# Kernel optimization log

Hardware: AMD Instinct MI355X
Metric: run time of the kernel (lower is better)

Reference implementation:

```python
import jax, jax.numpy as jnp
import numpy as np

B, N, C = 64, 16384, 3
NUM_PATCHES, PATCH_POINTS, EMBED_DIM = 64, 32, 384
BN_EPS = 1e-5


def farthest_point_sample(xyz, npoint):
    # xyz: (B, N, 3) -> (B, npoint) int32 indices. Deterministic start at index 0
    # (torch version uses a random start point).
    b, n, _ = xyz.shape
    bidx = jnp.arange(b)

    def step(carry, _):
        distance, farthest = carry
        centroid = xyz[bidx, farthest][:, None, :]          # (B,1,3)
        d = jnp.sum((xyz - centroid) ** 2, -1)              # (B,N)
        distance = jnp.minimum(distance, d)
        nxt = jnp.argmax(distance, -1).astype(jnp.int32)
        return (distance, nxt), farthest

    init = (jnp.full((b, n), 1e10, xyz.dtype), jnp.zeros((b,), jnp.int32))
    _, cent = jax.lax.scan(step, init, None, length=npoint)
    return jnp.transpose(cent)                               # (B, npoint)


def query_ball(xyz, new_xyz, nsample):
    # nsample nearest neighbors by squared distance (radius arg is unused in source).
    sq = (jnp.sum(new_xyz ** 2, -1)[:, :, None]
          + jnp.sum(xyz ** 2, -1)[:, None, :]
          - 2.0 * jnp.einsum('bsc,bnc->bsn', new_xyz, xyz))  # (B,S,N)
    _, idx = jax.lax.top_k(-sq, nsample)                     # smallest distances
    return idx                                               # (B,S,K)


def batchnorm(h, g, b):
    # training-mode BN over (batch*patches, points) per channel (last axis)
    m = jnp.mean(h, axis=(0, 1, 2))
    v = jnp.mean((h - m) ** 2, axis=(0, 1, 2))
    return (h - m) * jax.lax.rsqrt(v + BN_EPS) * g + b


def setup_inputs() -> dict:
    key = jax.random.key(0)
    ks = jax.random.split(key, 4)
    x = jax.random.normal(ks[0], (B, N, C), jnp.float32)
    W1 = jax.random.normal(ks[1], (64, C), jnp.float32) * (1.0 / np.sqrt(C))
    W2 = jax.random.normal(ks[2], (128, 64), jnp.float32) * (1.0 / np.sqrt(64))
    W3 = jax.random.normal(ks[3], (EMBED_DIM, 128), jnp.float32) * (1.0 / np.sqrt(128))
    return dict(
        x=x,
        W1=W1, b1=jnp.zeros((64,), jnp.float32),
        g1=jnp.ones((64,), jnp.float32), be1=jnp.zeros((64,), jnp.float32),
        W2=W2, b2=jnp.zeros((128,), jnp.float32),
        g2=jnp.ones((128,), jnp.float32), be2=jnp.zeros((128,), jnp.float32),
        W3=W3, b3=jnp.zeros((EMBED_DIM,), jnp.float32),
    )


def reference(x, W1, b1, g1, be1, W2, b2, g2, be2, W3, b3):
    b = x.shape[0]
    bidx2 = jnp.arange(b)[:, None]
    bidx3 = jnp.arange(b)[:, None, None]

    fps_idx = farthest_point_sample(x[:, :, :3], NUM_PATCHES)   # (B,S)
    centers = x[bidx2, fps_idx][:, :, :3]                       # (B,S,3)
    idx = query_ball(x[:, :, :3], centers, PATCH_POINTS)        # (B,S,K)
    patches = x[bidx3, idx]                                     # (B,S,K,C)
    patches = jnp.concatenate(
        [patches[..., :3] - centers[:, :, None, :], patches[..., 3:]], axis=-1)

    h = jnp.einsum('bskc,oc->bsko', patches, W1) + b1           # (B,S,K,64)
    h = jax.nn.relu(batchnorm(h, g1, be1))
    h = jnp.einsum('bsko,po->bskp', h, W2) + b2                 # (B,S,K,128)
    h = jax.nn.relu(batchnorm(h, g2, be2))
    h = jnp.einsum('bskp,ep->bske', h, W3) + b3                 # (B,S,K,384)
    embeddings = jnp.max(h, axis=2)                             # (B,S,384)
    return embeddings, centers
```

## Files before the change

kernel.cpp:

```cpp
#include <hip/hip_runtime.h>
#include <hip/hip_bf16.h>

#define B_  64
#define N_  16384
#define S_  64
#define K_  32
#define C1_ 64
#define C2_ 128
#define C3_ 384
#define R_  (B_*S_*K_)
#define BN_EPS_ 1e-5f

#define PATCH_OFF 0
#define CENT_OFF  (R_*3)
#define NB1_ 512
#define P1_OFF    (CENT_OFF + B_*S_*3)
#define SC1_OFF   (P1_OFF + NB1_*C1_*2)
#define NB2_ 512
#define P2_OFF    (SC1_OFF + 2*C1_)
#define SC2_OFF   (P2_OFF + NB2_*C2_*2)
#define W2BF_OFF  (SC2_OFF + 2*C2_)
#define W3BF_OFF  (W2BF_OFF + 4096)

#define MOMB_ 48

typedef short bf16x8 __attribute__((ext_vector_type(8)));
typedef float f32x4  __attribute__((ext_vector_type(4)));

static __device__ __forceinline__ unsigned short f2bf(float f) {
  unsigned u = __float_as_uint(f);
  unsigned r = (u + 0x7fffu + ((u >> 16) & 1u)) >> 16;
  return (unsigned short)r;
}

static __device__ __forceinline__ unsigned fToKey(float d) {
  unsigned u = __float_as_uint(d);
  return (u & 0x80000000u) ? ~u : (u | 0x80000000u);
}
static __device__ __forceinline__ float keyToF(unsigned k) {
  return (k & 0x80000000u) ? __uint_as_float(k & 0x7fffffffu)
                           : -__uint_as_float(~k);
}

__global__ void prep_kernel(const float* __restrict__ W2, const float* __restrict__ W3,
                            short* __restrict__ w2bf, short* __restrict__ w3bf) {
  int i = blockIdx.x * 256 + threadIdx.x;
  if (i < C2_*C1_) w2bf[i] = (short)f2bf(W2[i]);
  int j = i - C2_*C1_;
  if (j >= 0 && j < C3_*C2_) w3bf[j] = (short)f2bf(W3[j]);
}

__global__ __launch_bounds__(1024, 4) void fps_kernel(const float* __restrict__ x,
        float* __restrict__ centers, float* __restrict__ outCent) {
  int b = blockIdx.x;
  int t = threadIdx.x;
  const float* xb = x + (size_t)b * N_ * 3;
  float px[16], py[16], pz[16], dist[16];
#pragma unroll
  for (int j = 0; j < 16; ++j) {
    int n = j * 1024 + t;
    px[j] = xb[n*3+0]; py[j] = xb[n*3+1]; pz[j] = xb[n*3+2];
    dist[j] = 1e10f;
  }
  __shared__ float wd[2][16];
  __shared__ int   wi[2][16];
  float cx = xb[0], cy = xb[1], cz = xb[2];
  int lane = t & 63, wv = t >> 6;
  for (int s = 0; s < S_; ++s) {
    if (t == 0) {
      int task = b * S_ + s;
      centers[task*3+0] = cx; centers[task*3+1] = cy; centers[task*3+2] = cz;
      outCent[task*3+0] = cx; outCent[task*3+1] = cy; outCent[task*3+2] = cz;
    }
    float bd = -1.0f; int bn = 0;
#pragma unroll
    for (int j = 0; j < 16; ++j) {
      float dx = px[j]-cx, dy = py[j]-cy, dz = pz[j]-cz;
      float d = __builtin_fmaf(dz, dz, __builtin_fmaf(dy, dy, dx*dx));
      float dm = fminf(dist[j], d);
      dist[j] = dm;
      int n = j*1024 + t;
      if (dm > bd) { bd = dm; bn = n; }
    }
#pragma unroll
    for (int m = 1; m < 64; m <<= 1) {
      float od = __shfl_xor(bd, m, 64); int on = __shfl_xor(bn, m, 64);
      if (od > bd || (od == bd && on < bn)) { bd = od; bn = on; }
    }
    int buf = s & 1;
    if (lane == 0) { wd[buf][wv] = bd; wi[buf][wv] = bn; }
    __syncthreads();
    float vd = wd[buf][lane & 15];
    int   vi = wi[buf][lane & 15];
#pragma unroll
    for (int m = 1; m < 16; m <<= 1) {
      float od = __shfl_xor(vd, m, 64); int oi = __shfl_xor(vi, m, 64);
      if (od > vd || (od == vd && oi < vi)) { vd = od; vi = oi; }
    }
    int gn = vi;
    cx = xb[gn*3+0]; cy = xb[gn*3+1]; cz = xb[gn*3+2];
  }
}

__global__ __launch_bounds__(512, 4) void qb_kernel(const float* __restrict__ x,
        const float* __restrict__ centers, float* __restrict__ patches) {
  int t = threadIdx.x;
  int lane = t & 63, wv = t >> 6;
  int task = blockIdx.x;
  int b = task >> 6;
  const float* xb = x + (size_t)b * N_ * 3;
  float cx = centers[task*3+0], cy = centers[task*3+1], cz = centers[task*3+2];
  float A = __builtin_fmaf(cz, cz, __builtin_fmaf(cy, cy, cx*cx));

  __shared__ unsigned long long buf64[8][128];
  __shared__ unsigned long long wtop64[256];
  __shared__ int winIdx[32];
  __shared__ int sortedIdx[32];

  unsigned key[32];
  unsigned kmin = 0xffffffffu;
#pragma unroll
  for (int j = 0; j < 32; ++j) {
    int n = j * 512 + t;
    float qx = xb[n*3+0], qy = xb[n*3+1], qz = xb[n*3+2];
    float Bn = __builtin_fmaf(qz, qz, __builtin_fmaf(qy, qy, qx*qx));
    float dt = __builtin_fmaf(cz, qz, __builtin_fmaf(cy, qy, cx*qx));
    float d  = __builtin_fmaf(-2.0f, dt, A + Bn);
    unsigned u = __float_as_uint(d);
    unsigned k = (u & 0x80000000u) ? ~u : (u | 0x80000000u);
    key[j] = k;
    kmin = min(kmin, k);
  }
#pragma unroll
  for (int m = 1; m < 64; m <<= 1)
    kmin = min(kmin, (unsigned)__shfl_xor((int)kmin, m, 64));
  unsigned T0 = key[0];
#pragma unroll
  for (int m = 1; m < 64; m <<= 1)
    T0 = min(T0, (unsigned)__shfl_xor((int)T0, m, 64));

  unsigned Tcur = T0;
  int c;
  {
    int cc = 0;
#pragma unroll
    for (int j = 0; j < 32; ++j) cc += (key[j] < Tcur) ? 1 : 0;
#pragma unroll
    for (int m = 1; m < 64; m <<= 1) cc += __shfl_xor(cc, m, 64);
    c = cc;
  }
  float dmin = keyToF(kmin);
  for (int iter = 0; iter < 4 && !(c >= 32 && c <= 128); ++iter) {
    float dcur = keyToF(Tcur);
    if (!(dcur > dmin)) break;
    float cf = fmaxf((float)c, 1.0f);
    float ratio = exp2f(0.66666667f * log2f(64.0f / cf));
    float dnew = dmin + (dcur - dmin) * ratio;
    unsigned Tn = fToKey(dnew);
    if (Tn == Tcur) break;
    Tcur = Tn;
    int cc = 0;
#pragma unroll
    for (int j = 0; j < 32; ++j) cc += (key[j] < Tcur) ? 1 : 0;
#pragma unroll
    for (int m = 1; m < 64; m <<= 1) cc += __shfl_xor(cc, m, 64);
    c = cc;
  }

  int cW = 0;
  if (c >= 32 && c <= 128) {
    int base = 0;
#pragma unroll
    for (int j = 0; j < 32; ++j) {
      bool p = key[j] < Tcur;
      unsigned long long mk = __ballot(p);
      if (p) {
        int pos = base + (int)__popcll(mk & ((1ull << lane) - 1ull));
        buf64[wv][pos] = ((unsigned long long)key[j] << 32) | (unsigned)(j*512 + t);
      }
      base += (int)__popcll(mk);
    }
    cW = base;
  } else {
    unsigned a = 0xffffffffu, o = 0u;
#pragma unroll
    for (int j = 0; j < 32; ++j) { a &= key[j]; o |= key[j]; }
#pragma unroll
    for (int m = 1; m < 64; m <<= 1) {
      a &= (unsigned)__shfl_xor((int)a, m, 64);
      o |= (unsigned)__shfl_xor((int)o, m, 64);
    }
    unsigned diff = a ^ o;
    unsigned result = 0u, CAND = 0u;
    bool early = false;
    for (int bit = 31; bit >= 0; --bit) {
      unsigned msk = 1u << bit;
      if (!(diff & msk)) { result |= (a & msk); continue; }
      unsigned tryv = result | msk;
      int cc = 0;
#pragma unroll
      for (int j = 0; j < 32; ++j) cc += (key[j] < tryv) ? 1 : 0;
#pragma unroll
      for (int m = 1; m < 64; m <<= 1) cc += __shfl_xor(cc, m, 64);
      if (cc >= 32 && cc <= 128) { early = true; CAND = tryv; break; }
      if (cc < 32) result = tryv;
    }
    if (early) {
      int base = 0;
#pragma unroll
      for (int j = 0; j < 32; ++j) {
        bool p = key[j] < CAND;
        unsigned long long mk = __ballot(p);
        if (p) {
          int pos = base + (int)__popcll(mk & ((1ull << lane) - 1ull));
          buf64[wv][pos] = ((unsigned long long)key[j] << 32) | (unsigned)(j*512 + t);
        }
        base += (int)__popcll(mk);
      }
      cW = base;
    } else {
      unsigned T = result;
      int base = 0;
#pragma unroll
      for (int j = 0; j < 32; ++j) {
        bool p = key[j] < T;
        unsigned long long mk = __ballot(p);
        if (p) {
          int pos = base + (int)__popcll(mk & ((1ull << lane) - 1ull));
          buf64[wv][pos] = ((unsigned long long)key[j] << 32) | (unsigned)(j*512 + t);
        }
        base += (int)__popcll(mk);
      }
      int cl = base;
      int picked = -1;
      for (int r = 0; r < 32 - cl; ++r) {
        int cand = 0x7fffffff;
#pragma unroll
        for (int j = 0; j < 32; ++j) {
          int n = j*512 + t;
          if (key[j] == T && n > picked && n < cand) cand = n;
        }
#pragma unroll
        for (int m = 1; m < 64; m <<= 1) cand = min(cand, __shfl_xor(cand, m, 64));
        if (lane == 0)
          buf64[wv][cl + r] = ((unsigned long long)T << 32) | (unsigned)cand;
        picked = cand;
      }
      cW = 32;
    }
  }

  {
    unsigned long long my0 = (lane < cW) ? buf64[wv][lane] : ~0ull;
    unsigned long long my1 = (lane + 64 < cW) ? buf64[wv][lane + 64] : ~0ull;
    int r0 = 0, r1 = 0;
    for (int jj = 0; jj < cW; ++jj) {
      unsigned long long ov = buf64[wv][jj];
      r0 += (ov < my0) ? 1 : 0;
      r1 += (ov < my1) ? 1 : 0;
    }
    if (lane < cW && r0 < 32) wtop64[wv*32 + r0] = my0;
    if (lane + 64 < cW && r1 < 32) wtop64[wv*32 + r1] = my1;
  }
  __syncthreads();

  if (t < 256) {
    unsigned long long me = wtop64[t];
    int rk = 0;
    for (int jj = 0; jj < 256; ++jj) rk += (wtop64[jj] < me) ? 1 : 0;
    if (rk < 32) winIdx[rk] = (int)(me & 0xffffffffu);
  }
  __syncthreads();
  if (t < 32) {
    int v = winIdx[t];
    int slot = 0;
#pragma unroll
    for (int j = 0; j < 32; ++j) slot += (winIdx[j] < v) ? 1 : 0;
    sortedIdx[slot] = v;
  }
  __syncthreads();
  if (t < 32) {
    int n = sortedIdx[t];
    float qx = xb[n*3+0], qy = xb[n*3+1], qz = xb[n*3+2];
    size_t row = (size_t)task * K_ + t;
    patches[row*3+0] = qx - cx;
    patches[row*3+1] = qy - cy;
    patches[row*3+2] = qz - cz;
  }
}

__global__ __launch_bounds__(256) void mom_kernel(const float* __restrict__ patches,
        float* __restrict__ mom) {
  int t = threadIdx.x;
  float s[9] = {0,0,0,0,0,0,0,0,0};
  for (int r = blockIdx.x*256 + t; r < R_; r += MOMB_*256) {
    const float* p = patches + (size_t)r*3;
    float x0 = p[0], y0 = p[1], z0 = p[2];
    s[0] += x0; s[1] += y0; s[2] += z0;
    s[3] += x0*x0; s[4] += y0*y0; s[5] += z0*z0;
    s[6] += x0*y0; s[7] += x0*z0; s[8] += y0*z0;
  }
  __shared__ float red[4][9];
  int lane = t & 63, wv = t >> 6;
#pragma unroll
  for (int k = 0; k < 9; ++k) {
    float v = s[k];
#pragma unroll
    for (int m = 1; m < 64; m <<= 1) v += __shfl_xor(v, m, 64);
    if (lane == 0) red[wv][k] = v;
  }
  __syncthreads();
  if (t < 9) mom[blockIdx.x*9 + t] = red[0][t] + red[1][t] + red[2][t] + red[3][t];
}

__global__ void finalize1_kernel(const float* __restrict__ mom,
        const float* __restrict__ W1, const float* __restrict__ b1,
        const float* __restrict__ g, const float* __restrict__ be,
        float* __restrict__ scale, float* __restrict__ shift) {
  int o = threadIdx.x;
  __shared__ double M[9];
  if (o < 9) {
    double ss = 0.0;
    for (int i = 0; i < MOMB_; ++i) ss += (double)mom[i*9 + o];
    M[o] = ss;
  }
  __syncthreads();
  if (o >= C1_) return;
  double w0 = W1[o*3], w1 = W1[o*3+1], w2 = W1[o*3+2], bb = b1[o];
  double wSp = w0*M[0] + w1*M[1] + w2*M[2];
  double s1 = wSp + (double)R_*bb;
  double s2 = w0*w0*M[3] + w1*w1*M[4] + w2*w2*M[5]
            + 2.0*(w0*w1*M[6] + w0*w2*M[7] + w1*w2*M[8])
            + 2.0*bb*wSp + (double)R_*bb*bb;
  float m   = (float)(s1 / (double)R_);
  float eh2 = (float)(s2 / (double)R_);
  float v = eh2 - m*m;
  float rs = rsqrtf(v + BN_EPS_);
  float sc = g[o] * rs;
  scale[o] = sc;
  shift[o] = be[o] - m*sc;
}

__global__ void finalize_kernel(const float* __restrict__ part, int nblk, int nch,
        const float* __restrict__ g, const float* __restrict__ be,
        const float* __restrict__ bias,
        float* __restrict__ scale, float* __restrict__ shift) {
  int o = threadIdx.x;
  if (o >= nch) return;
  double s1 = 0.0, s2 = 0.0;
  for (int i = 0; i < nblk; ++i) {
    s1 += (double)part[i*nch*2 + o*2 + 0];
    s2 += (double)part[i*nch*2 + o*2 + 1];
  }
  float m   = (float)(s1 / (double)R_);
  float eh2 = (float)(s2 / (double)R_);
  float v = eh2 - m*m;
  float rs = rsqrtf(v + BN_EPS_);
  float sc = g[o] * rs;
  scale[o] = sc;
  float sh = be[o] - m*sc;
  if (bias) sh += bias[o]*sc;
  shift[o] = sh;
}

__global__ __launch_bounds__(256) void stats2_kernel(const float* __restrict__ patches,
        const float* __restrict__ W1, const float* __restrict__ b1,
        const float* __restrict__ sc1, const float* __restrict__ sh1,
        const float* __restrict__ W2, const float* __restrict__ b2,
        float* __restrict__ part) {
  __shared__ float a1L[128][68];
  __shared__ float red[2][128][2];
  int t = threadIdx.x;
  float4 wreg[16];
  const float4* w2r = (const float4*)(W2 + (t & 127)*64);
#pragma unroll
  for (int c = 0; c < 16; ++c) wreg[c] = w2r[c];
  float bb = b2[t & 127];
  float s1 = 0.f, s2 = 0.f;
  int rg = t >> 7;
  for (int tile = 0; tile < 2; ++tile) {
    int r0 = blockIdx.x * 256 + tile * 128;
    {
      int r = t & 127, oh = t >> 7;
      const float* p = patches + (size_t)(r0 + r) * 3;
      float p0 = p[0], p1 = p[1], p2 = p[2];
#pragma unroll
      for (int j = 0; j < 32; ++j) {
        int o = oh*32 + j;
        float h = p0*W1[o*3] + p1*W1[o*3+1] + p2*W1[o*3+2] + b1[o];
        a1L[r][o] = fmaxf(h*sc1[o] + sh1[o], 0.f);
      }
    }
    __syncthreads();
    for (int i = 0; i < 64; ++i) {
      int r = rg*64 + i;
      float acc = bb;
      const float4* a4 = (const float4*)(&a1L[r][0]);
#pragma unroll
      for (int c = 0; c < 16; ++c) {
        float4 a = a4[c];
        acc += a.x*wreg[c].x; acc += a.y*wreg[c].y;
        acc += a.z*wreg[c].z; acc += a.w*wreg[c].w;
      }
      s1 += acc; s2 += acc*acc;
    }
    __syncthreads();
  }
  red[rg][t & 127][0] = s1; red[rg][t & 127][1] = s2;
  __syncthreads();
  if (t < 128) {
    part[blockIdx.x*256 + t*2 + 0] = red[0][t][0] + red[1][t][0];
    part[blockIdx.x*256 + t*2 + 1] = red[0][t][1] + red[1][t][1];
  }
}

__global__ __launch_bounds__(256) void embed_kernel(
        const float* __restrict__ patches,
        const float* __restrict__ W1, const float* __restrict__ b1,
        const float* __restrict__ sc1, const float* __restrict__ sh1,
        const short* __restrict__ w2bf, const float* __restrict__ sc2,
        const float* __restrict__ sh2f,
        const short* __restrict__ w3bf, const float* __restrict__ b3,
        float* __restrict__ out) {
  __shared__ char lds[49152];
  int t = threadIdx.x;
  int l = t & 63, w = t >> 6;
  int lo = l & 15, hi = l >> 4;

  {
    int row = t >> 1, half = t & 1;
    const float* p = patches + ((size_t)blockIdx.x*128 + row)*3;
    float p0 = p[0], p1 = p[1], p2 = p[2];
    int swz = (row & 7) << 4;
    char* dst = lds + row*128;
#pragma unroll
    for (int g = 0; g < 4; ++g) {
      unsigned short pk[8];
#pragma unroll
      for (int j = 0; j < 8; ++j) {
        int o = half*32 + g*8 + j;
        float h = p0*W1[o*3] + p1*W1[o*3+1] + p2*W1[o*3+2] + b1[o];
        pk[j] = f2bf(fmaxf(h*sc1[o] + sh1[o], 0.f));
      }
      int4 v;
      v.x = pk[0] | (pk[1]<<16); v.y = pk[2] | (pk[3]<<16);
      v.z = pk[4] | (pk[5]<<16); v.w = pk[6] | (pk[7]<<16);
      *(int4*)(dst + (((half*64 + g*16)) ^ swz)) = v;
    }
  }
  __syncthreads();

  {
    bf16x8 af[2][2];
#pragma unroll
    for (int mt = 0; mt < 2; ++mt) {
      int row = w*32 + mt*16 + lo;
#pragma unroll
      for (int ks = 0; ks < 2; ++ks)
        af[mt][ks] = *(const bf16x8*)(lds + row*128 + ((ks*64 + hi*16) ^ ((row&7)<<4)));
    }
#pragma unroll
    for (int nt = 0; nt < 8; ++nt) {
      f32x4 acc0 = {0.f,0.f,0.f,0.f}, acc1 = {0.f,0.f,0.f,0.f};
      int n = nt*16 + lo;
#pragma unroll
      for (int ks = 0; ks < 2; ++ks) {
        bf16x8 bfv = *(const bf16x8*)(w2bf + n*64 + ks*32 + hi*8);
        acc0 = __builtin_amdgcn_mfma_f32_16x16x32_bf16(af[0][ks], bfv, acc0, 0, 0, 0);
        acc1 = __builtin_amdgcn_mfma_f32_16x16x32_bf16(af[1][ks], bfv, acc1, 0, 0, 0);
      }
      float sc = sc2[n], sh = sh2f[n];
#pragma unroll
      for (int mt = 0; mt < 2; ++mt) {
        f32x4 c = mt ? acc1 : acc0;
#pragma unroll
        for (int r = 0; r < 4; ++r) {
          int row = w*32 + mt*16 + hi*4 + r;
          unsigned short v = f2bf(fmaxf(c[r]*sc + sh, 0.f));
          *(short*)(lds + 16384 + row*256 + ((n*2) ^ ((row&7)<<4))) = (short)v;
        }
      }
    }
  }
  __syncthreads();

  {
    bf16x8 af[2][4];
#pragma unroll
    for (int mt = 0; mt < 2; ++mt) {
      int row = w*32 + mt*16 + lo;
#pragma unroll
      for (int ks = 0; ks < 4; ++ks)
        af[mt][ks] = *(const bf16x8*)(lds + 16384 + row*256 + ((ks*64 + hi*16) ^ ((row&7)<<4)));
    }
    size_t gtask = (size_t)blockIdx.x*4 + w;
#pragma unroll 4
    for (int nt = 0; nt < 24; ++nt) {
      f32x4 acc0 = {0.f,0.f,0.f,0.f}, acc1 = {0.f,0.f,0.f,0.f};
      int e = nt*16 + lo;
#pragma unroll
      for (int ks = 0; ks < 4; ++ks) {
        bf16x8 bfv = *(const bf16x8*)(w3bf + e*128 + ks*32 + hi*8);
        acc0 = __builtin_amdgcn_mfma_f32_16x16x32_bf16(af[0][ks], bfv, acc0, 0, 0, 0);
        acc1 = __builtin_amdgcn_mfma_f32_16x16x32_bf16(af[1][ks], bfv, acc1, 0, 0, 0);
      }
      float m0 = fmaxf(fmaxf(acc0[0], acc0[1]), fmaxf(acc0[2], acc0[3]));
      float m1 = fmaxf(fmaxf(acc1[0], acc1[1]), fmaxf(acc1[2], acc1[3]));
      float m = fmaxf(m0, m1);
      m = fmaxf(m, __shfl_xor(m, 16, 64));
      m = fmaxf(m, __shfl_xor(m, 32, 64));
      if (l < 16) out[gtask*C3_ + e] = m + b3[e];
    }
  }
}

extern "C" void kernel_launch(void* const* d_in, const int* in_sizes, int n_in,
                              void* d_out, int out_size, void* d_ws, size_t ws_size,
                              hipStream_t stream) {
  (void)in_sizes; (void)n_in; (void)out_size; (void)ws_size;
  const float* x   = (const float*)d_in[0];
  const float* W1  = (const float*)d_in[1];
  const float* b1  = (const float*)d_in[2];
  const float* g1  = (const float*)d_in[3];
  const float* be1 = (const float*)d_in[4];
  const float* W2  = (const float*)d_in[5];
  const float* b2  = (const float*)d_in[6];
  const float* g2  = (const float*)d_in[7];
  const float* be2 = (const float*)d_in[8];
  const float* W3  = (const float*)d_in[9];
  const float* b3  = (const float*)d_in[10];
  float* out = (float*)d_out;
  float* ws  = (float*)d_ws;

  float* patches = ws + PATCH_OFF;
  float* centers = ws + CENT_OFF;
  float* mom1    = ws + P1_OFF;
  float* sc1     = ws + SC1_OFF; float* sh1 = sc1 + C1_;
  float* part2   = ws + P2_OFF;
  float* sc2     = ws + SC2_OFF; float* sh2 = sc2 + C2_;
  short* w2bf    = (short*)(ws + W2BF_OFF);
  short* w3bf    = (short*)(ws + W3BF_OFF);
  float* outCent = out + (size_t)B_*S_*C3_;

  prep_kernel<<<dim3((C2_*C1_ + C3_*C2_)/256), dim3(256), 0, stream>>>(W2, W3, w2bf, w3bf);
  fps_kernel<<<dim3(B_), dim3(1024), 0, stream>>>(x, centers, outCent);
  qb_kernel<<<dim3(4096), dim3(512), 0, stream>>>(x, centers, patches);
  mom_kernel<<<dim3(MOMB_), dim3(256), 0, stream>>>(patches, mom1);
  finalize1_kernel<<<dim3(1), dim3(64), 0, stream>>>(mom1, W1, b1, g1, be1, sc1, sh1);
  stats2_kernel<<<dim3(NB2_), dim3(256), 0, stream>>>(patches, W1, b1, sc1, sh1, W2, b2, part2);
  finalize_kernel<<<dim3(1), dim3(128), 0, stream>>>(part2, NB2_, C2_, g2, be2, b2, sc2, sh2);
  embed_kernel<<<dim3(1024), dim3(256), 0, stream>>>(patches, W1, b1, sc1, sh1,
                                                     w2bf, sc2, sh2, w3bf, b3, out);
}
```

Baseline: 634.4 us.

## Use block-wide threshold selection in query-ball kernel with 1024 threads

```diff
diff --git a/kernel.cpp b/kernel.cpp
--- a/kernel.cpp
+++ b/kernel.cpp
@@ -102,7 +102,7 @@
   }
 }
 
-__global__ __launch_bounds__(512, 4) void qb_kernel(const float* __restrict__ x,
+__global__ __launch_bounds__(1024, 4) void qb_kernel(const float* __restrict__ x,
         const float* __restrict__ centers, float* __restrict__ patches) {
   int t = threadIdx.x;
   int lane = t & 63, wv = t >> 6;
@@ -112,45 +112,57 @@
   float cx = centers[task*3+0], cy = centers[task*3+1], cz = centers[task*3+2];
   float A = __builtin_fmaf(cz, cz, __builtin_fmaf(cy, cy, cx*cx));
 
-  __shared__ unsigned long long buf64[8][128];
-  __shared__ unsigned long long wtop64[256];
+  __shared__ unsigned wred[16];
+  __shared__ unsigned wred2[16];
+  __shared__ int cwv[16];
+  __shared__ unsigned long long cand[128];
   __shared__ int winIdx[32];
   __shared__ int sortedIdx[32];
 
-  unsigned key[32];
-  unsigned kmin = 0xffffffffu;
-#pragma unroll
-  for (int j = 0; j < 32; ++j) {
-    int n = j * 512 + t;
+  unsigned key[16];
+  unsigned kmin = 0xffffffffu, ksam = 0xffffffffu;
+#pragma unroll
+  for (int j = 0; j < 16; ++j) {
+    int n = j * 1024 + t;
     float qx = xb[n*3+0], qy = xb[n*3+1], qz = xb[n*3+2];
     float Bn = __builtin_fmaf(qz, qz, __builtin_fmaf(qy, qy, qx*qx));
     float dt = __builtin_fmaf(cz, qz, __builtin_fmaf(cy, qy, cx*qx));
     float d  = __builtin_fmaf(-2.0f, dt, A + Bn);
-    unsigned u = __float_as_uint(d);
-    unsigned k = (u & 0x80000000u) ? ~u : (u | 0x80000000u);
+    unsigned k = fToKey(d);
     key[j] = k;
     kmin = min(kmin, k);
   }
-#pragma unroll
-  for (int m = 1; m < 64; m <<= 1)
+  if ((lane & 3) == 0) ksam = key[0];
+#pragma unroll
+  for (int m = 1; m < 64; m <<= 1) {
     kmin = min(kmin, (unsigned)__shfl_xor((int)kmin, m, 64));
-  unsigned T0 = key[0];
-#pragma unroll
-  for (int m = 1; m < 64; m <<= 1)
-    T0 = min(T0, (unsigned)__shfl_xor((int)T0, m, 64));
+    ksam = min(ksam, (unsigned)__shfl_xor((int)ksam, m, 64));
+  }
+  if (lane == 0) { wred[wv] = kmin; wred2[wv] = ksam; }
+  __syncthreads();
+  unsigned gmin = wred[0], T0 = wred2[0];
+#pragma unroll
+  for (int w = 1; w < 16; ++w) { gmin = min(gmin, wred[w]); T0 = min(T0, wred2[w]); }
+
+  auto countLess = [&](unsigned T) -> int {
+    int cc = 0;
+#pragma unroll
+    for (int j = 0; j < 16; ++j) cc += (key[j] < T) ? 1 : 0;
+#pragma unroll
+    for (int m = 1; m < 64; m <<= 1) cc += __shfl_xor(cc, m, 64);
+    __syncthreads();
+    if (lane == 0) wred[wv] = (unsigned)cc;
+    __syncthreads();
+    int tot = 0;
+#pragma unroll
+    for (int w = 0; w < 16; ++w) tot += (int)wred[w];
+    return tot;
+  };
 
   unsigned Tcur = T0;
-  int c;
-  {
-    int cc = 0;
-#pragma unroll
-    for (int j = 0; j < 32; ++j) cc += (key[j] < Tcur) ? 1 : 0;
-#pragma unroll
-    for (int m = 1; m < 64; m <<= 1) cc += __shfl_xor(cc, m, 64);
-    c = cc;
-  }
-  float dmin = keyToF(kmin);
-  for (int iter = 0; iter < 4 && !(c >= 32 && c <= 128); ++iter) {
+  int c = countLess(Tcur);
+  float dmin = keyToF(gmin);
+  for (int iter = 0; iter < 3 && !(c >= 32 && c <= 128); ++iter) {
     float dcur = keyToF(Tcur);
     if (!(dcur > dmin)) break;
     float cf = fmaxf((float)c, 1.0f);
@@ -159,115 +171,92 @@
     unsigned Tn = fToKey(dnew);
     if (Tn == Tcur) break;
     Tcur = Tn;
-    int cc = 0;
-#pragma unroll
-    for (int j = 0; j < 32; ++j) cc += (key[j] < Tcur) ? 1 : 0;
-#pragma unroll
-    for (int m = 1; m < 64; m <<= 1) cc += __shfl_xor(cc, m, 64);
-    c = cc;
-  }
-
-  int cW = 0;
-  if (c >= 32 && c <= 128) {
+    c = countLess(Tcur);
+  }
+
+  auto compactLess = [&](unsigned T) -> int {
+    int wc = 0;
+#pragma unroll
+    for (int j = 0; j < 16; ++j)
+      wc += (int)__popcll(__ballot(key[j] < T));
+    __syncthreads();
+    if (lane == 0) cwv[wv] = wc;
+    __syncthreads();
     int base = 0;
-#pragma unroll
-    for (int j = 0; j < 32; ++j) {
-      bool p = key[j] < Tcur;
+    for (int w = 0; w < wv; ++w) base += cwv[w];
+    int tot = 0;
+#pragma unroll
+    for (int w = 0; w < 16; ++w) tot += cwv[w];
+    int p2 = base;
+#pragma unroll
+    for (int j = 0; j < 16; ++j) {
+      bool p = key[j] < T;
       unsigned long long mk = __ballot(p);
       if (p) {
-        int pos = base + (int)__popcll(mk & ((1ull << lane) - 1ull));
-        buf64[wv][pos] = ((unsigned long long)key[j] << 32) | (unsigned)(j*512 + t);
-      }
-      base += (int)__popcll(mk);
-    }
-    cW = base;
+        int pos = p2 + (int)__popcll(mk & ((1ull << lane) - 1ull));
+        cand[pos] = ((unsigned long long)key[j] << 32) | (unsigned)(j*1024 + t);
+      }
+      p2 += (int)__popcll(mk);
+    }
+    return tot;
+  };
+
+  int ctot;
+  if (c >= 32 && c <= 128) {
+    ctot = compactLess(Tcur);
   } else {
     unsigned a = 0xffffffffu, o = 0u;
 #pragma unroll
-    for (int j = 0; j < 32; ++j) { a &= key[j]; o |= key[j]; }
+    for (int j = 0; j < 16; ++j) { a &= key[j]; o |= key[j]; }
 #pragma unroll
     for (int m = 1; m < 64; m <<= 1) {
       a &= (unsigned)__shfl_xor((int)a, m, 64);
       o |= (unsigned)__shfl_xor((int)o, m, 64);
     }
-    unsigned diff = a ^ o;
-    unsigned result = 0u, CAND = 0u;
-    bool early = false;
+    __syncthreads();
+    if (lane == 0) { wred[wv] = a; wred2[wv] = o; }
+    __syncthreads();
+    unsigned gA = wred[0], gO = wred2[0];
+#pragma unroll
+    for (int w = 1; w < 16; ++w) { gA &= wred[w]; gO |= wred2[w]; }
+    unsigned diff = gA ^ gO;
+    unsigned result = 0u;
     for (int bit = 31; bit >= 0; --bit) {
       unsigned msk = 1u << bit;
-      if (!(diff & msk)) { result |= (a & msk); continue; }
-      unsigned tryv = result | msk;
-      int cc = 0;
-#pragma unroll
-      for (int j = 0; j < 32; ++j) cc += (key[j] < tryv) ? 1 : 0;
-#pragma unroll
-      for (int m = 1; m < 64; m <<= 1) cc += __shfl_xor(cc, m, 64);
-      if (cc >= 32 && cc <= 128) { early = true; CAND = tryv; break; }
-      if (cc < 32) result = tryv;
-    }
-    if (early) {
-      int base = 0;
-#pragma unroll
-      for (int j = 0; j < 32; ++j) {
-        bool p = key[j] < CAND;
-        unsigned long long mk = __ballot(p);
-        if (p) {
-          int pos = base + (int)__popcll(mk & ((1ull << lane) - 1ull));
-          buf64[wv][pos] = ((unsigned long long)key[j] << 32) | (unsigned)(j*512 + t);
-        }
-        base += (int)__popcll(mk);
-      }
-      cW = base;
-    } else {
-      unsigned T = result;
-      int base = 0;
-#pragma unroll
-      for (int j = 0; j < 32; ++j) {
-        bool p = key[j] < T;
-        unsigned long long mk = __ballot(p);
-        if (p) {
-          int pos = base + (int)__popcll(mk & ((1ull << lane) - 1ull));
-          buf64[wv][pos] = ((unsigned long long)key[j] << 32) | (unsigned)(j*512 + t);
-        }
-        base += (int)__popcll(mk);
-      }
-      int cl = base;
-      int picked = -1;
-      for (int r = 0; r < 32 - cl; ++r) {
-        int cand = 0x7fffffff;
-#pragma unroll
-        for (int j = 0; j < 32; ++j) {
-          int n = j*512 + t;
-          if (key[j] == T && n > picked && n < cand) cand = n;
-        }
-#pragma unroll
-        for (int m = 1; m < 64; m <<= 1) cand = min(cand, __shfl_xor(cand, m, 64));
-        if (lane == 0)
-          buf64[wv][cl + r] = ((unsigned long long)T << 32) | (unsigned)cand;
-        picked = cand;
-      }
-      cW = 32;
-    }
-  }
-
-  {
-    unsigned long long my0 = (lane < cW) ? buf64[wv][lane] : ~0ull;
-    unsigned long long my1 = (lane + 64 < cW) ? buf64[wv][lane + 64] : ~0ull;
-    int r0 = 0, r1 = 0;
-    for (int jj = 0; jj < cW; ++jj) {
-      unsigned long long ov = buf64[wv][jj];
-      r0 += (ov < my0) ? 1 : 0;
-      r1 += (ov < my1) ? 1 : 0;
-    }
-    if (lane < cW && r0 < 32) wtop64[wv*32 + r0] = my0;
-    if (lane + 64 < cW && r1 < 32) wtop64[wv*32 + r1] = my1;
-  }
-  __syncthreads();
-
-  if (t < 256) {
-    unsigned long long me = wtop64[t];
+      if (!(diff & msk)) { result |= (gA & msk); continue; }
+      if (countLess(result | msk) < 32) result |= msk;
+    }
+    unsigned Tx = result;
+    int cl = compactLess(Tx);
+    int need = 32 - cl;
+    int picked = -1;
+    for (int r = 0; r < need; ++r) {
+      int candn = 0x7fffffff;
+#pragma unroll
+      for (int j = 0; j < 16; ++j) {
+        int n = j*1024 + t;
+        if (key[j] == Tx && n > picked && n < candn) candn = n;
+      }
+#pragma unroll
+      for (int m = 1; m < 64; m <<= 1) candn = min(candn, __shfl_xor(candn, m, 64));
+      __syncthreads();
+      if (lane == 0) wred[wv] = (unsigned)candn;
+      __syncthreads();
+      unsigned wmin = wred[0];
+#pragma unroll
+      for (int w = 1; w < 16; ++w) wmin = min(wmin, wred[w]);
+      int winner = (int)wmin;
+      if (t == 0) cand[cl + r] = ((unsigned long long)Tx << 32) | (unsigned)winner;
+      picked = winner;
+    }
+    ctot = 32;
+  }
+  __syncthreads();
+
+  if (t < ctot) {
+    unsigned long long me = cand[t];
     int rk = 0;
-    for (int jj = 0; jj < 256; ++jj) rk += (wtop64[jj] < me) ? 1 : 0;
+    for (int j = 0; j < ctot; ++j) rk += (cand[j] < me) ? 1 : 0;
     if (rk < 32) winIdx[rk] = (int)(me & 0xffffffffu);
   }
   __syncthreads();
@@ -544,7 +533,7 @@
 
   prep_kernel<<<dim3((C2_*C1_ + C3_*C2_)/256), dim3(256), 0, stream>>>(W2, W3, w2bf, w3bf);
   fps_kernel<<<dim3(B_), dim3(1024), 0, stream>>>(x, centers, outCent);
-  qb_kernel<<<dim3(4096), dim3(512), 0, stream>>>(x, centers, patches);
+  qb_kernel<<<dim3(4096), dim3(1024), 0, stream>>>(x, centers, patches);
   mom_kernel<<<dim3(MOMB_), dim3(256), 0, stream>>>(patches, mom1);
   finalize1_kernel<<<dim3(1), dim3(64), 0, stream>>>(mom1, W1, b1, g1, be1, sc1, sh1);
   stats2_kernel<<<dim3(NB2_), dim3(256), 0, stream>>>(patches, W1, b1, sc1, sh1, W2, b2, part2);
```

New measurement: 824.8 us. 30.0% more time.
